# Optimization experiments

Measured on AMD Instinct MI355X. Metric: run time of the kernel, lower is better.

The kernel has to match this reference:

```python
import jax, jax.numpy as jnp
import numpy as np

COST_CLASS = 1.0
COST_POLYLINE = 1.0
COST_DIRECTION = 1.0
EPS = 1e-6


def setup_inputs() -> dict:
    key = jax.random.key(0)
    k1, k2, k3, k4 = jax.random.split(key, 4)
    bs, Q, C, P, T = 2, 256, 16, 20, 256
    return {
        "pred_logits": jax.random.normal(k1, (bs, Q, C), dtype=jnp.float32),
        "pred_polylines": jax.random.normal(k2, (bs, Q, P, 2), dtype=jnp.float32),
        "tgt_labels": jax.random.randint(k3, (T,), 0, C),
        "tgt_polylines": jax.random.normal(k4, (T, P, 2), dtype=jnp.float32),
    }


def reference(pred_logits, pred_polylines, tgt_labels, tgt_polylines):
    # pred_logits: [bs, Q, C]; pred_polylines: [bs, Q, P, 2]
    # tgt_labels: [T]; tgt_polylines: [T, P, 2]
    bs, Q = pred_logits.shape[:2]
    out_prob = jax.nn.softmax(pred_logits.reshape(bs * Q, -1), axis=-1)  # [N, C]
    out_poly = pred_polylines.reshape(bs * Q, *pred_polylines.shape[2:])  # [N, P, 2]

    # classification cost: -p(tgt_class)  -> [N, T]
    cost_class = -out_prob[:, tgt_labels]

    # pairwise polyline L1 cdist, all pairs at once: d[n, t, p, q]
    d = (jnp.abs(out_poly[:, None, :, None, 0] - tgt_polylines[None, :, None, :, 0])
         + jnp.abs(out_poly[:, None, :, None, 1] - tgt_polylines[None, :, None, :, 1]))
    # bidirectional average-of-min distance (Chamfer-style), averaged -> [N, T]
    min1 = d.min(axis=3).mean(axis=2)  # pred -> gt
    min2 = d.min(axis=2).mean(axis=2)  # gt -> pred
    cost_polyline = (min1 + min2) / 2

    # direction cost: 1 - cos(start->end vectors)
    pd = out_poly[:, -1] - out_poly[:, 0]          # [N, 2]
    gd = tgt_polylines[:, -1] - tgt_polylines[:, 0]  # [T, 2]
    pd = pd / (jnp.linalg.norm(pd, axis=-1, keepdims=True) + EPS)
    gd = gd / (jnp.linalg.norm(gd, axis=-1, keepdims=True) + EPS)
    cost_direction = 1.0 - pd @ gd.T               # [N, T]

    C = (COST_CLASS * cost_class
         + COST_POLYLINE * cost_polyline
         + COST_DIRECTION * cost_direction)
    return C.reshape(bs, Q, -1)
```

## Files before the change

### kernel.cpp

```cpp
#include <hip/hip_runtime.h>
#include <math.h>

#define BS    2
#define NQ    256
#define NCLS  16
#define NP    20
#define NT    256
#define NN    (BS * NQ)
#define FEPS  1e-6f
#define QPL   5
#define TPB   128
#define PHALF 10
#define THREADS (TPB * 4)

__global__ __launch_bounds__(THREADS) void matcher_cost_kernel(
    const float* __restrict__ logits,
    const float* __restrict__ ppoly,
    const int*   __restrict__ tlabels,
    const float* __restrict__ tpoly,
    float*       __restrict__ out)
{
    const int bid   = blockIdx.x;
    const int n     = bid >> 1;
    const int tbase = (bid & 1) * TPB;
    const int tid   = threadIdx.x;
    const int t     = tbase + (tid >> 2);
    const int z     = tid & 3;

    __shared__ float2 s_pxy[NP];
    __shared__ float  s_prob[NCLS];
    __shared__ float  s_invden;
    __shared__ float  s_dir[2];

    if (tid < NP * 2) ((float*)s_pxy)[tid] = ppoly[n * NP * 2 + tid];
    if (tid < NCLS) {
        const float* lp = logits + n * NCLS;
        float mx = lp[0];
        #pragma unroll
        for (int c = 1; c < NCLS; ++c) mx = fmaxf(fmaxf(mx, lp[c]), mx);
        s_prob[tid] = __expf(lp[tid] - mx);
    }
    __syncthreads();
    if (tid == 0) {
        float den = 0.f;
        #pragma unroll
        for (int c = 0; c < NCLS; ++c) den += s_prob[c];
        s_invden = 1.f / den;
        float2 a = s_pxy[0], b = s_pxy[NP - 1];
        float dx = b.x - a.x, dy = b.y - a.y;
        float nrm = sqrtf(dx * dx + dy * dy) + FEPS;
        s_dir[0] = dx / nrm; s_dir[1] = dy / nrm;
    }

    float tx[QPL], ty[QPL], m2[QPL];
    {
        const float* tp = &tpoly[(t * NP + z * QPL) * 2];
        float4 a = *reinterpret_cast<const float4*>(tp);
        float4 b = *reinterpret_cast<const float4*>(tp + 4);
        float2 c = *reinterpret_cast<const float2*>(tp + 8);
        tx[0] = a.x; ty[0] = a.y; tx[1] = a.z; ty[1] = a.w;
        tx[2] = b.x; ty[2] = b.y; tx[3] = b.z; ty[3] = b.w;
        tx[4] = c.x; ty[4] = c.y;
        #pragma unroll
        for (int k = 0; k < QPL; ++k) m2[k] = 1e30f;
    }

    float sum1 = 0.f;
    #pragma unroll
    for (int h = 0; h < 2; ++h) {
        float m1a[PHALF];
        #pragma unroll
        for (int pp = 0; pp < PHALF; ++pp) {
            const float2 pxy = s_pxy[h * PHALF + pp];
            const float d0 = fabsf(pxy.x - tx[0]) + fabsf(pxy.y - ty[0]);
            const float d1 = fabsf(pxy.x - tx[1]) + fabsf(pxy.y - ty[1]);
            const float d2 = fabsf(pxy.x - tx[2]) + fabsf(pxy.y - ty[2]);
            const float d3 = fabsf(pxy.x - tx[3]) + fabsf(pxy.y - ty[3]);
            const float d4 = fabsf(pxy.x - tx[4]) + fabsf(pxy.y - ty[4]);
            m2[0] = fminf(m2[0], d0);
            m2[1] = fminf(m2[1], d1);
            m2[2] = fminf(m2[2], d2);
            m2[3] = fminf(m2[3], d3);
            m2[4] = fminf(m2[4], d4);
            const float a01 = fminf(fminf(d0, d1), d2);
            m1a[pp] = fminf(fminf(a01, d3), d4);
        }
        float s = 0.f;
        #pragma unroll
        for (int pp = 0; pp < PHALF; ++pp) {
            float v = m1a[pp];
            v = fminf(v, __shfl_xor(v, 1, 4));
            v = fminf(v, __shfl_xor(v, 2, 4));
            s += v;
        }
        sum1 += s;
    }
    float sum2 = ((m2[0] + m2[1]) + (m2[2] + m2[3])) + m2[4];
    sum2 += __shfl_xor(sum2, 1, 4);
    sum2 += __shfl_xor(sum2, 2, 4);
    const float cost_poly = (sum1 + sum2) * (0.5f / (float)NP);

    const float g1x = __shfl_xor(tx[QPL - 1], 3, 4);
    const float g1y = __shfl_xor(ty[QPL - 1], 3, 4);

    if (z == 0) {
        const int lbl = tlabels[t];
        const float cost_class = -s_prob[lbl] * s_invden;

        const float gdx = g1x - tx[0];
        const float gdy = g1y - ty[0];
        const float gn = sqrtf(gdx * gdx + gdy * gdy) + FEPS;
        const float cost_dir = 1.f - (s_dir[0] * gdx + s_dir[1] * gdy) / gn;

        out[n * NT + t] = cost_class + cost_poly + cost_dir;
    }
}

extern "C" void kernel_launch(void* const* d_in, const int* in_sizes, int n_in,
                              void* d_out, int out_size, void* d_ws, size_t ws_size,
                              hipStream_t stream) {
    const float* logits  = (const float*)d_in[0];
    const float* ppoly   = (const float*)d_in[1];
    const int*   tlabels = (const int*)d_in[2];
    const float* tpoly   = (const float*)d_in[3];
    float*       out     = (float*)d_out;

    matcher_cost_kernel<<<dim3(NN * (NT / TPB)), dim3(THREADS), 0, stream>>>(
        logits, ppoly, tlabels, tpoly, out);
}
```

Measured before the change: 13.28 us.

## Compute polyline L1 distances in packed fp16 with two threads per target

Result: no change. 13.38 us (+0.8%).

```diff
diff --git a/kernel.cpp b/kernel.cpp
--- a/kernel.cpp
+++ b/kernel.cpp
@@ -8,10 +8,12 @@
 #define NT    256
 #define NN    (BS * NQ)
 #define FEPS  1e-6f
-#define QPL   5
 #define TPB   128
-#define PHALF 10
-#define THREADS (TPB * 4)
+#define THREADS (TPB * 2)
+#define QPL   10
+#define NPK   5
+
+typedef _Float16 h2 __attribute__((ext_vector_type(2)));
 
 __global__ __launch_bounds__(THREADS) void matcher_cost_kernel(
     const float* __restrict__ logits,
@@ -24,93 +26,102 @@
     const int n     = bid >> 1;
     const int tbase = (bid & 1) * TPB;
     const int tid   = threadIdx.x;
-    const int t     = tbase + (tid >> 2);
-    const int z     = tid & 3;
+    const int t     = tbase + (tid >> 1);
+    const int z     = tid & 1;
 
-    __shared__ float2 s_pxy[NP];
-    __shared__ float  s_prob[NCLS];
-    __shared__ float  s_invden;
-    __shared__ float  s_dir[2];
+    __shared__ uint2 s_h[NP];
+    __shared__ float s_prob[NCLS];
+    __shared__ float s_invden;
+    __shared__ float s_dir2[2];
 
-    if (tid < NP * 2) ((float*)s_pxy)[tid] = ppoly[n * NP * 2 + tid];
+    const int lbl = tlabels[t];
+
+    if (tid < NP) {
+        float2 v = *reinterpret_cast<const float2*>(&ppoly[n * NP * 2 + 2 * tid]);
+        h2 hx = { (_Float16)v.x, (_Float16)v.x };
+        h2 hy = { (_Float16)v.y, (_Float16)v.y };
+        s_h[tid] = make_uint2(__builtin_bit_cast(unsigned, hx),
+                              __builtin_bit_cast(unsigned, hy));
+    }
     if (tid < NCLS) {
         const float* lp = logits + n * NCLS;
         float mx = lp[0];
         #pragma unroll
-        for (int c = 1; c < NCLS; ++c) mx = fmaxf(fmaxf(mx, lp[c]), mx);
+        for (int c = 1; c < NCLS; ++c) mx = fmaxf(mx, lp[c]);
         s_prob[tid] = __expf(lp[tid] - mx);
     }
-    __syncthreads();
     if (tid == 0) {
         float den = 0.f;
         #pragma unroll
         for (int c = 0; c < NCLS; ++c) den += s_prob[c];
         s_invden = 1.f / den;
-        float2 a = s_pxy[0], b = s_pxy[NP - 1];
+        float2 a = *reinterpret_cast<const float2*>(&ppoly[n * NP * 2]);
+        float2 b = *reinterpret_cast<const float2*>(&ppoly[n * NP * 2 + 2 * (NP - 1)]);
         float dx = b.x - a.x, dy = b.y - a.y;
         float nrm = sqrtf(dx * dx + dy * dy) + FEPS;
-        s_dir[0] = dx / nrm; s_dir[1] = dy / nrm;
+        s_dir2[0] = dx / nrm; s_dir2[1] = dy / nrm;
+    }
+    __syncthreads();
+
+    h2 tx[NPK], ty[NPK], m2[NPK];
+    float ex0, ey0, exL, eyL;
+    {
+        const float* tp = &tpoly[(t * NP + z * QPL) * 2];
+        #pragma unroll
+        for (int j = 0; j < NPK; ++j) {
+            float4 v = *reinterpret_cast<const float4*>(tp + 4 * j);
+            tx[j] = (h2){ (_Float16)v.x, (_Float16)v.z };
+            ty[j] = (h2){ (_Float16)v.y, (_Float16)v.w };
+            m2[j] = (h2){ (_Float16)65504.f, (_Float16)65504.f };
+            if (j == 0)       { ex0 = v.x; ey0 = v.y; }
+            if (j == NPK - 1) { exL = v.z; eyL = v.w; }
+        }
     }
 
-    float tx[QPL], ty[QPL], m2[QPL];
-    {
-        const float* tp = &tpoly[(t * NP + z * QPL) * 2];
-        float4 a = *reinterpret_cast<const float4*>(tp);
-        float4 b = *reinterpret_cast<const float4*>(tp + 4);
-        float2 c = *reinterpret_cast<const float2*>(tp + 8);
-        tx[0] = a.x; ty[0] = a.y; tx[1] = a.z; ty[1] = a.w;
-        tx[2] = b.x; ty[2] = b.y; tx[3] = b.z; ty[3] = b.w;
-        tx[4] = c.x; ty[4] = c.y;
+    float m1f[NP];
+    #pragma unroll
+    for (int p = 0; p < NP; ++p) {
+        const uint2 hh = s_h[p];
+        const h2 hx = __builtin_bit_cast(h2, hh.x);
+        const h2 hy = __builtin_bit_cast(h2, hh.y);
+        h2 dmin;
         #pragma unroll
-        for (int k = 0; k < QPL; ++k) m2[k] = 1e30f;
+        for (int j = 0; j < NPK; ++j) {
+            h2 dx = hx - tx[j];
+            dx = __builtin_elementwise_max(dx, -dx);
+            h2 dy = hy - ty[j];
+            dy = __builtin_elementwise_max(dy, -dy);
+            h2 d = dx + dy;
+            m2[j] = __builtin_elementwise_min(m2[j], d);
+            dmin = (j == 0) ? d : __builtin_elementwise_min(dmin, d);
+        }
+        m1f[p] = fminf((float)dmin.x, (float)dmin.y);
     }
 
     float sum1 = 0.f;
     #pragma unroll
-    for (int h = 0; h < 2; ++h) {
-        float m1a[PHALF];
-        #pragma unroll
-        for (int pp = 0; pp < PHALF; ++pp) {
-            const float2 pxy = s_pxy[h * PHALF + pp];
-            const float d0 = fabsf(pxy.x - tx[0]) + fabsf(pxy.y - ty[0]);
-            const float d1 = fabsf(pxy.x - tx[1]) + fabsf(pxy.y - ty[1]);
-            const float d2 = fabsf(pxy.x - tx[2]) + fabsf(pxy.y - ty[2]);
-            const float d3 = fabsf(pxy.x - tx[3]) + fabsf(pxy.y - ty[3]);
-            const float d4 = fabsf(pxy.x - tx[4]) + fabsf(pxy.y - ty[4]);
-            m2[0] = fminf(m2[0], d0);
-            m2[1] = fminf(m2[1], d1);
-            m2[2] = fminf(m2[2], d2);
-            m2[3] = fminf(m2[3], d3);
-            m2[4] = fminf(m2[4], d4);
-            const float a01 = fminf(fminf(d0, d1), d2);
-            m1a[pp] = fminf(fminf(a01, d3), d4);
-        }
-        float s = 0.f;
-        #pragma unroll
-        for (int pp = 0; pp < PHALF; ++pp) {
-            float v = m1a[pp];
-            v = fminf(v, __shfl_xor(v, 1, 4));
-            v = fminf(v, __shfl_xor(v, 2, 4));
-            s += v;
-        }
-        sum1 += s;
+    for (int p = 0; p < NP; ++p) {
+        float v = m1f[p];
+        v = fminf(v, __shfl_xor(v, 1, 2));
+        sum1 += v;
     }
-    float sum2 = ((m2[0] + m2[1]) + (m2[2] + m2[3])) + m2[4];
-    sum2 += __shfl_xor(sum2, 1, 4);
-    sum2 += __shfl_xor(sum2, 2, 4);
+    float sum2 = 0.f;
+    #pragma unroll
+    for (int j = 0; j < NPK; ++j)
+        sum2 += (float)m2[j].x + (float)m2[j].y;
+    sum2 += __shfl_xor(sum2, 1, 2);
     const float cost_poly = (sum1 + sum2) * (0.5f / (float)NP);
 
-    const float g1x = __shfl_xor(tx[QPL - 1], 3, 4);
-    const float g1y = __shfl_xor(ty[QPL - 1], 3, 4);
+    const float g1x = __shfl_xor(exL, 1, 2);
+    const float g1y = __shfl_xor(eyL, 1, 2);
 
     if (z == 0) {
-        const int lbl = tlabels[t];
         const float cost_class = -s_prob[lbl] * s_invden;
 
-        const float gdx = g1x - tx[0];
-        const float gdy = g1y - ty[0];
+        const float gdx = g1x - ex0;
+        const float gdy = g1y - ey0;
         const float gn = sqrtf(gdx * gdx + gdy * gdy) + FEPS;
-        const float cost_dir = 1.f - (s_dir[0] * gdx + s_dir[1] * gdy) / gn;
+        const float cost_dir = 1.f - (s_dir2[0] * gdx + s_dir2[1] * gdy) / gn;
 
         out[n * NT + t] = cost_class + cost_poly + cost_dir;
     }
```
